# Performance work log

Hardware: AMD Instinct MI355X
Metric: run time of the kernel (lower is better)

Reference implementation:

```python
import jax, jax.numpy as jnp
import numpy as np

N, E = 100000, 3200000
IN, HID, OUT = 512, 256, 64
K, ALPHA = 10, 0.1


def setup_inputs() -> dict:
    key = jax.random.key(0)
    k1, k2, k3, k4, k5, k6 = jax.random.split(key, 6)
    x = jax.random.normal(k1, (N, IN), dtype=jnp.float32)
    edge_index = jax.random.randint(k2, (2, E), 0, N, dtype=jnp.int64)
    s1 = 1.0 / np.sqrt(IN)
    s2 = 1.0 / np.sqrt(HID)
    # nn.Linear default init: U(-1/sqrt(fan_in), 1/sqrt(fan_in))
    W1 = jax.random.uniform(k3, (IN, HID), jnp.float32, -s1, s1)
    b1 = jax.random.uniform(k4, (HID,), jnp.float32, -s1, s1)
    W2 = jax.random.uniform(k5, (HID, OUT), jnp.float32, -s2, s2)
    b2 = jax.random.uniform(k6, (OUT,), jnp.float32, -s2, s2)
    return {"x": x, "edge_index": edge_index, "W1": W1, "b1": b1, "W2": W2, "b2": b2}


def reference(x, edge_index, W1, b1, W2, b2):
    # MLP (dropout is identity in eval mode)
    h = jax.nn.relu(x @ W1 + b1) @ W2 + b2  # [N, OUT]

    # gcn_norm with self-loops (PyG APPNP default, normalize=True)
    loop = jnp.arange(N, dtype=edge_index.dtype)
    src = jnp.concatenate([edge_index[0], loop])  # message sources
    dst = jnp.concatenate([edge_index[1], loop])  # aggregation targets
    deg = jax.ops.segment_sum(jnp.ones_like(dst, dtype=h.dtype), dst, num_segments=N)
    dinv = jnp.where(deg > 0, jax.lax.rsqrt(jnp.maximum(deg, 1.0)), 0.0)
    norm = (dinv[src] * dinv[dst])[:, None]  # [E+N, 1]

    x0 = h
    def step(hk, _):
        agg = jax.ops.segment_sum(norm * hk[src], dst, num_segments=N)
        return (1.0 - ALPHA) * agg + ALPHA * x0, None

    h, _ = jax.lax.scan(step, h, None, length=K)
    return h
```

## Files before the change

### kernel.cpp

```cpp
#include <hip/hip_runtime.h>
#include <hip/hip_bf16.h>

#define IN_F  512
#define HID_F 256
#define OUT_F 64

#define BSHIFT 9
#define BNODES 512
#define NBK_MAX 256
#define EBUF_CAP 18432
#define CURS 16
#define CHUNK 8192

typedef __attribute__((ext_vector_type(8))) short bf16x8;
typedef __attribute__((ext_vector_type(4))) float f32x4;

__device__ inline unsigned short f2bf(float f) {
    unsigned u = __float_as_uint(f);
    u += 0x7FFFu + ((u >> 16) & 1u);
    return (unsigned short)(u >> 16);
}
__device__ inline float bf2f(unsigned v) {
    return __uint_as_float(v << 16);
}

__device__ inline bf16x8 cvt8(f32x4 v0, f32x4 v1) {
    bf16x8 r;
    r[0] = (short)f2bf(v0[0]); r[1] = (short)f2bf(v0[1]);
    r[2] = (short)f2bf(v0[2]); r[3] = (short)f2bf(v0[3]);
    r[4] = (short)f2bf(v1[0]); r[5] = (short)f2bf(v1[1]);
    r[6] = (short)f2bf(v1[2]); r[7] = (short)f2bf(v1[3]);
    return r;
}

__device__ inline void gload_lds16(const void* g, void* l) {
    __builtin_amdgcn_global_load_lds(
        (const __attribute__((address_space(1))) void*)g,
        (__attribute__((address_space(3))) void*)l, 16, 0, 0);
}

__global__ void prep_w_kernel(const float* __restrict__ W1,
                              const float* __restrict__ W2,
                              unsigned short* __restrict__ W1T,
                              unsigned short* __restrict__ W2T)
{
    int i = blockIdx.x * 256 + threadIdx.x;
    if (i < IN_F * HID_F) {
        int k = i / HID_F, n = i % HID_F;
        W1T[n * IN_F + k] = f2bf(W1[i]);
    }
    if (i < HID_F * OUT_F) {
        int k = i / OUT_F, n = i % OUT_F;
        W2T[n * HID_F + k] = f2bf(W2[i]);
    }
}

__global__ __launch_bounds__(512, 4) void mlp_kernel(
    const float* __restrict__ x, const unsigned short* __restrict__ W1T,
    const float* __restrict__ b1, const unsigned short* __restrict__ W2T,
    const float* __restrict__ b2, const float* __restrict__ dinv,
    unsigned short* __restrict__ h0bf, unsigned short* __restrict__ g0, int N)
{
    __shared__ uint4 smem4[4096];
    char* smem = (char*)smem4;

    const int t  = threadIdx.x;
    const int w  = t >> 6;
    const int l  = t & 63;
    const int lr = l & 15;
    const int lq = l >> 4;
    const int wr = w & 3;
    const int wc = w >> 2;

    const int row0 = blockIdx.x * 128;

    f32x4 acc[2][8];
    #pragma unroll
    for (int s = 0; s < 2; ++s)
        #pragma unroll
        for (int f = 0; f < 8; ++f) acc[s][f] = (f32x4){0.f, 0.f, 0.f, 0.f};

    const int ar0 = row0 + wr * 32 + lr;
    const int ar1 = ar0 + 16;
    const bool av0 = ar0 < N, av1 = ar1 < N;
    const float* xp0 = x + (size_t)ar0 * IN_F + lq * 8;
    const float* xp1 = x + (size_t)ar1 * IN_F + lq * 8;

    auto stage = [&](int ks, int buf) {
        #pragma unroll
        for (int is = 0; is < 4; ++is) {
            int j  = is * 512 + t;
            int n  = j >> 3;
            int cs = (j & 7) ^ (n & 7);
            const unsigned short* srcp = W1T + (size_t)n * IN_F + ks * 64 + cs * 8;
            char* dstp = smem + buf * 32768 + is * 8192 + (t >> 6) * 1024;
            gload_lds16(srcp, dstp);
        }
    };

    stage(0, 0);
    __syncthreads();

    for (int ks = 0; ks < 8; ++ks) {
        if (ks < 7) stage(ks + 1, (ks + 1) & 1);
        const char* bb = smem + (ks & 1) * 32768;
        #pragma unroll
        for (int kh = 0; kh < 2; ++kh) {
            const int kofs = ks * 64 + kh * 32;
            bf16x8 a0v, a1v;
            if (av0) {
                a0v = cvt8(*(const f32x4*)(xp0 + kofs),
                           *(const f32x4*)(xp0 + kofs + 4));
            } else {
                #pragma unroll
                for (int j = 0; j < 8; ++j) a0v[j] = 0;
            }
            if (av1) {
                a1v = cvt8(*(const f32x4*)(xp1 + kofs),
                           *(const f32x4*)(xp1 + kofs + 4));
            } else {
                #pragma unroll
                for (int j = 0; j < 8; ++j) a1v[j] = 0;
            }
            #pragma unroll
            for (int f = 0; f < 8; ++f) {
                int n = wc * 128 + f * 16 + lr;
                unsigned off = (unsigned)(n * 128 + kh * 64 + lq * 16);
                bf16x8 b = *(const bf16x8*)(bb + (off ^ ((unsigned)(n & 7) << 4)));
                acc[0][f] = __builtin_amdgcn_mfma_f32_16x16x32_bf16(a0v, b, acc[0][f], 0, 0, 0);
                acc[1][f] = __builtin_amdgcn_mfma_f32_16x16x32_bf16(a1v, b, acc[1][f], 0, 0, 0);
            }
        }
        __syncthreads();
    }

    #pragma unroll
    for (int f = 0; f < 8; ++f) {
        int c = wc * 128 + f * 16 + lr;
        float bbv = b1[c];
        #pragma unroll
        for (int sub = 0; sub < 2; ++sub) {
            #pragma unroll
            for (int j2 = 0; j2 < 4; ++j2) {
                int rr = wr * 32 + sub * 16 + lq * 4 + j2;
                float vv = acc[sub][f][j2] + bbv;
                vv = vv > 0.f ? vv : 0.f;
                unsigned off = (unsigned)(rr * 512 + c * 2);
                *(unsigned short*)(smem + (off ^ ((unsigned)(rr & 7) << 4))) = f2bf(vv);
            }
        }
    }
    __syncthreads();

    const int ct = w & 3;
    const int rh = w >> 2;
    f32x4 a2[4];
    #pragma unroll
    for (int m = 0; m < 4; ++m) a2[m] = (f32x4){0.f, 0.f, 0.f, 0.f};

    const unsigned short* w2p = W2T + (size_t)(ct * 16 + lr) * HID_F + lq * 8;

    #pragma unroll 2
    for (int ks = 0; ks < 8; ++ks) {
        bf16x8 bfrag = *(const bf16x8*)(w2p + ks * 32);
        #pragma unroll
        for (int m = 0; m < 4; ++m) {
            int rr = rh * 64 + m * 16 + lr;
            unsigned off = (unsigned)(rr * 512 + ks * 64 + lq * 16);
            bf16x8 afrag = *(const bf16x8*)(smem + (off ^ ((unsigned)(rr & 7) << 4)));
            a2[m] = __builtin_amdgcn_mfma_f32_16x16x32_bf16(afrag, bfrag, a2[m], 0, 0, 0);
        }
    }

    float bb2 = b2[ct * 16 + lr];
    #pragma unroll
    for (int m = 0; m < 4; ++m) {
        #pragma unroll
        for (int j2 = 0; j2 < 4; ++j2) {
            int rr = row0 + rh * 64 + m * 16 + lq * 4 + j2;
            if (rr < N) {
                float v = a2[m][j2] + bb2;
                int c = ct * 16 + lr;
                h0bf[(size_t)rr * OUT_F + c] = f2bf(v);
                g0[(size_t)rr * OUT_F + c]   = f2bf(dinv[rr] * v);
            }
        }
    }
}

__global__ __launch_bounds__(256) void binned_scatter_kernel(
    const int* __restrict__ src, const int* __restrict__ dst,
    int* __restrict__ bcur, unsigned* __restrict__ ebuf, int E, int nbk)
{
    __shared__ int hist[NBK_MAX];
    __shared__ int gbase[NBK_MAX];
    __shared__ int lcur[NBK_MAX];

    const int t  = threadIdx.x;
    const int bs = blockIdx.x * CHUNK;
    const int nE = min(CHUNK, E - bs);

    if (t < NBK_MAX) { hist[t] = 0; lcur[t] = 0; }
    __syncthreads();

    for (int j = t; j < nE; j += 256)
        atomicAdd(&hist[dst[bs + j] >> BSHIFT], 1);
    __syncthreads();

    for (int b = t; b < nbk; b += 256)
        gbase[b] = hist[b] ? atomicAdd(&bcur[b * CURS], hist[b]) : 0;
    __syncthreads();

    for (int j = t; j < nE; j += 256) {
        int d = dst[bs + j];
        int s = src[bs + j];
        int b = d >> BSHIFT;
        int r = atomicAdd(&lcur[b], 1);
        unsigned pos = (unsigned)(gbase[b] + r);
        if (pos < EBUF_CAP)
            ebuf[(size_t)b * EBUF_CAP + pos] =
                ((unsigned)(d & (BNODES - 1)) << 17) | (unsigned)s;
    }
}

__global__ __launch_bounds__(1024) void bucket_scan_kernel(
    const int* __restrict__ bcur, int* __restrict__ bbase,
    int* __restrict__ off, int nbk, int N, int E)
{
    __shared__ int sm[1024];
    int t = threadIdx.x;
    int v = 0;
    if (t < nbk) {
        v = bcur[t * CURS];
        if (v > EBUF_CAP) v = EBUF_CAP;
    }
    sm[t] = v;
    __syncthreads();
    for (int ofs = 1; ofs < 1024; ofs <<= 1) {
        int x = (t >= ofs) ? sm[t - ofs] : 0;
        __syncthreads();
        sm[t] += x;
        __syncthreads();
    }
    if (t < nbk) bbase[t] = sm[t] - v;
    if (t == nbk - 1) bbase[nbk] = sm[t];
    if (t == 0) off[N] = E;
}

__global__ __launch_bounds__(256) void bucket_build_kernel(
    const unsigned* __restrict__ ebuf, const int* __restrict__ bbase,
    float* __restrict__ dinv, int* __restrict__ off,
    int* __restrict__ csr, int N)
{
    __shared__ int cnt[BNODES];
    __shared__ int loc[BNODES];
    __shared__ int tsum[256];
    const int b = blockIdx.x;
    const int t = threadIdx.x;
    const int beg = bbase[b];
    const int nE  = bbase[b + 1] - beg;
    const unsigned* eb = ebuf + (size_t)b * EBUF_CAP;

    cnt[t] = 0; cnt[t + 256] = 0;
    __syncthreads();
    for (int j = t; j < nE; j += 256)
        atomicAdd(&cnt[eb[j] >> 17], 1);
    __syncthreads();

    int c0 = cnt[2 * t], c1 = cnt[2 * t + 1];
    tsum[t] = c0 + c1;
    __syncthreads();
    for (int ofs = 1; ofs < 256; ofs <<= 1) {
        int v = (t >= ofs) ? tsum[t - ofs] : 0;
        __syncthreads();
        tsum[t] += v;
        __syncthreads();
    }
    int base = (t == 0) ? 0 : tsum[t - 1];
    loc[2 * t]     = beg + base;
    loc[2 * t + 1] = beg + base + c0;
    __syncthreads();

    for (int u = t; u < BNODES; u += 256) {
        int node = b * BNODES + u;
        if (node < N) {
            dinv[node] = rsqrtf((float)(cnt[u] + 1));
            off[node]  = loc[u];
        }
    }
    __syncthreads();
    for (int j = t; j < nE; j += 256) {
        unsigned u = eb[j];
        int pos = atomicAdd(&loc[u >> 17], 1);
        csr[pos] = (int)(u & 0x1FFFFu);
    }
}

__global__ __launch_bounds__(256) void step_kernel(
    const unsigned short* __restrict__ gin,
    const unsigned short* __restrict__ h0bf,
    unsigned short* __restrict__ gout, float* __restrict__ outf,
    const int* __restrict__ off, const int* __restrict__ csr,
    const float* __restrict__ dinv, int N, int last)
{
    const int t    = threadIdx.x;
    const int wid  = (blockIdx.x * 256 + t) >> 6;
    if (wid >= N) return;
    const int lane = t & 63;
    const int es   = lane >> 3;
    const int fb   = lane & 7;

    const uint4* gin4 = (const uint4*)gin;

    float a0 = 0.f, a1 = 0.f, a2 = 0.f, a3 = 0.f;
    float a4 = 0.f, a5 = 0.f, a6 = 0.f, a7 = 0.f;
    const int beg = __builtin_amdgcn_readfirstlane(off[wid]);
    const int end = __builtin_amdgcn_readfirstlane(off[wid + 1]);

    for (int i = beg; i < end; i += 32) {
        int idx[4];
        #pragma unroll
        for (int jj = 0; jj < 4; ++jj) {
            int e = i + jj * 8 + es;
            idx[jj] = (e < end) ? csr[e] : -1;
        }
        uint4 v[4];
        #pragma unroll
        for (int jj = 0; jj < 4; ++jj) {
            v[jj] = (idx[jj] >= 0) ? gin4[(size_t)idx[jj] * 8 + fb]
                                   : make_uint4(0u, 0u, 0u, 0u);
        }
        #pragma unroll
        for (int jj = 0; jj < 4; ++jj) {
            a0 += bf2f(v[jj].x & 0xffffu);
            a1 += bf2f(v[jj].x >> 16);
            a2 += bf2f(v[jj].y & 0xffffu);
            a3 += bf2f(v[jj].y >> 16);
            a4 += bf2f(v[jj].z & 0xffffu);
            a5 += bf2f(v[jj].z >> 16);
            a6 += bf2f(v[jj].w & 0xffffu);
            a7 += bf2f(v[jj].w >> 16);
        }
    }

    a0 += __shfl_xor(a0, 8); a0 += __shfl_xor(a0, 16); a0 += __shfl_xor(a0, 32);
    a1 += __shfl_xor(a1, 8); a1 += __shfl_xor(a1, 16); a1 += __shfl_xor(a1, 32);
    a2 += __shfl_xor(a2, 8); a2 += __shfl_xor(a2, 16); a2 += __shfl_xor(a2, 32);
    a3 += __shfl_xor(a3, 8); a3 += __shfl_xor(a3, 16); a3 += __shfl_xor(a3, 32);
    a4 += __shfl_xor(a4, 8); a4 += __shfl_xor(a4, 16); a4 += __shfl_xor(a4, 32);
    a5 += __shfl_xor(a5, 8); a5 += __shfl_xor(a5, 16); a5 += __shfl_xor(a5, 32);
    a6 += __shfl_xor(a6, 8); a6 += __shfl_xor(a6, 16); a6 += __shfl_xor(a6, 32);
    a7 += __shfl_xor(a7, 8); a7 += __shfl_xor(a7, 16); a7 += __shfl_xor(a7, 32);

    if (es == 0) {
        uint4 sv = gin4[(size_t)wid * 8 + fb];
        uint4 hv = ((const uint4*)h0bf)[(size_t)wid * 8 + fb];
        float dv = dinv[wid];
        float s0 = a0 + bf2f(sv.x & 0xffffu);
        float s1 = a1 + bf2f(sv.x >> 16);
        float s2 = a2 + bf2f(sv.y & 0xffffu);
        float s3 = a3 + bf2f(sv.y >> 16);
        float s4 = a4 + bf2f(sv.z & 0xffffu);
        float s5 = a5 + bf2f(sv.z >> 16);
        float s6 = a6 + bf2f(sv.w & 0xffffu);
        float s7 = a7 + bf2f(sv.w >> 16);
        float r0 = 0.9f * dv * s0 + 0.1f * bf2f(hv.x & 0xffffu);
        float r1 = 0.9f * dv * s1 + 0.1f * bf2f(hv.x >> 16);
        float r2 = 0.9f * dv * s2 + 0.1f * bf2f(hv.y & 0xffffu);
        float r3 = 0.9f * dv * s3 + 0.1f * bf2f(hv.y >> 16);
        float r4 = 0.9f * dv * s4 + 0.1f * bf2f(hv.z & 0xffffu);
        float r5 = 0.9f * dv * s5 + 0.1f * bf2f(hv.z >> 16);
        float r6 = 0.9f * dv * s6 + 0.1f * bf2f(hv.w & 0xffffu);
        float r7 = 0.9f * dv * s7 + 0.1f * bf2f(hv.w >> 16);
        if (last) {
            float* op = outf + (size_t)wid * OUT_F + fb * 8;
            *(float4*)op       = make_float4(r0, r1, r2, r3);
            *(float4*)(op + 4) = make_float4(r4, r5, r6, r7);
        } else {
            uint4 g;
            g.x = (unsigned)f2bf(dv * r0) | ((unsigned)f2bf(dv * r1) << 16);
            g.y = (unsigned)f2bf(dv * r2) | ((unsigned)f2bf(dv * r3) << 16);
            g.z = (unsigned)f2bf(dv * r4) | ((unsigned)f2bf(dv * r5) << 16);
            g.w = (unsigned)f2bf(dv * r6) | ((unsigned)f2bf(dv * r7) << 16);
            ((uint4*)gout)[(size_t)wid * 8 + fb] = g;
        }
    }
}

extern "C" void kernel_launch(void* const* d_in, const int* in_sizes, int n_in,
                              void* d_out, int out_size, void* d_ws, size_t ws_size,
                              hipStream_t stream)
{
    const float* x  = (const float*)d_in[0];
    const int*   ei = (const int*)d_in[1];
    const float* W1 = (const float*)d_in[2];
    const float* b1 = (const float*)d_in[3];
    const float* W2 = (const float*)d_in[4];
    const float* b2 = (const float*)d_in[5];
    float* out = (float*)d_out;

    const int N = in_sizes[0] / IN_F;
    const int E = in_sizes[1] / 2;
    const int* src = ei;
    const int* dst = ei + E;
    const int nbk = (N + BNODES - 1) >> BSHIFT;

    char* wsp = (char*)d_ws;
    auto alloc = [&](size_t bytes) -> char* {
        char* p = wsp;
        wsp += (bytes + 255) & ~(size_t)255;
        return p;
    };
    int*   off  = (int*)  alloc((size_t)(N + 1) * 4);
    float* dinv = (float*)alloc((size_t)N * 4);
    int*   csr  = (int*)  alloc((size_t)E * 4);
    unsigned* ebuf = (unsigned*)alloc((size_t)nbk * EBUF_CAP * 4);
    int*   bcur  = (int*) alloc((size_t)nbk * CURS * 4);
    int*   bbase = (int*) alloc((size_t)(nbk + 1) * 4);
    unsigned short* h0bf = (unsigned short*)alloc((size_t)N * OUT_F * 2);
    unsigned short* gA   = (unsigned short*)alloc((size_t)N * OUT_F * 2);
    unsigned short* gB   = (unsigned short*)alloc((size_t)N * OUT_F * 2);
    unsigned short* W1T  = (unsigned short*)alloc((size_t)IN_F * HID_F * 2);
    unsigned short* W2T  = (unsigned short*)alloc((size_t)HID_F * OUT_F * 2);

    hipMemsetAsync(bcur, 0, (size_t)nbk * CURS * 4, stream);

    const int gScat = (E + CHUNK - 1) / CHUNK;
    binned_scatter_kernel<<<gScat, 256, 0, stream>>>(src, dst, bcur, ebuf, E, nbk);
    bucket_scan_kernel<<<1, 1024, 0, stream>>>(bcur, bbase, off, nbk, N, E);
    bucket_build_kernel<<<nbk, 256, 0, stream>>>(ebuf, bbase, dinv, off, csr, N);

    prep_w_kernel<<<(IN_F * HID_F + 255) / 256, 256, 0, stream>>>(W1, W2, W1T, W2T);
    mlp_kernel<<<(N + 127) / 128, 512, 0, stream>>>(x, W1T, b1, W2T, b2, dinv,
                                                    h0bf, gA, N);

    const int gS = (N + 3) / 4;
    const unsigned short* gin = gA;
    unsigned short* gout = gB;
    for (int k = 0; k < 10; ++k) {
        int last = (k == 9);
        step_kernel<<<gS, 256, 0, stream>>>(gin, h0bf, gout, out, off, csr,
                                            dinv, N, last);
        const unsigned short* tmp = gin;
        gin = gout;
        gout = (unsigned short*)tmp;
    }
}
```

Measured before the change: 765.0 us.

## Stage x tiles through LDS with async loads alongside W1 in first GEMM

The first MLP GEMM used to read x straight from global memory into registers inside the k-loop, while only W1 was staged through LDS. The new code stages both the fp32 x tile and the bf16 W1 tile into double-buffered LDS with asynchronous global-to-LDS loads and swizzled layouts, using a k-step of 32 over 16 iterations. The aim is to overlap the large x stream with MFMA work and hide global load latency. The cost is more barriers, more LDS traffic, and clamped row reads for out-of-range rows in place of zeroing.

Result: faster. 736.0 us (-3.8%).

```diff
diff --git a/kernel.cpp b/kernel.cpp
--- a/kernel.cpp
+++ b/kernel.cpp
@@ -80,56 +80,55 @@
         #pragma unroll
         for (int f = 0; f < 8; ++f) acc[s][f] = (f32x4){0.f, 0.f, 0.f, 0.f};
 
-    const int ar0 = row0 + wr * 32 + lr;
-    const int ar1 = ar0 + 16;
-    const bool av0 = ar0 < N, av1 = ar1 < N;
-    const float* xp0 = x + (size_t)ar0 * IN_F + lq * 8;
-    const float* xp1 = x + (size_t)ar1 * IN_F + lq * 8;
-
-    auto stage = [&](int ks, int buf) {
-        #pragma unroll
-        for (int is = 0; is < 4; ++is) {
-            int j  = is * 512 + t;
-            int n  = j >> 3;
-            int cs = (j & 7) ^ (n & 7);
-            const unsigned short* srcp = W1T + (size_t)n * IN_F + ks * 64 + cs * 8;
-            char* dstp = smem + buf * 32768 + is * 8192 + (t >> 6) * 1024;
+    auto stageX = [&](int ks, int buf) {
+        #pragma unroll
+        for (int is = 0; is < 2; ++is) {
+            int j = is * 512 + t;
+            int r = j >> 3;
+            int c = j & 7;
+            int gr = row0 + r; if (gr > N - 1) gr = N - 1;
+            const float* srcp = x + (size_t)gr * IN_F + ks * 32 + ((c ^ (r & 7)) << 2);
+            char* dstp = smem + buf * 16384 + is * 8192 + (t >> 6) * 1024;
             gload_lds16(srcp, dstp);
         }
     };
-
-    stage(0, 0);
-    __syncthreads();
-
-    for (int ks = 0; ks < 8; ++ks) {
-        if (ks < 7) stage(ks + 1, (ks + 1) & 1);
-        const char* bb = smem + (ks & 1) * 32768;
-        #pragma unroll
-        for (int kh = 0; kh < 2; ++kh) {
-            const int kofs = ks * 64 + kh * 32;
-            bf16x8 a0v, a1v;
-            if (av0) {
-                a0v = cvt8(*(const f32x4*)(xp0 + kofs),
-                           *(const f32x4*)(xp0 + kofs + 4));
-            } else {
-                #pragma unroll
-                for (int j = 0; j < 8; ++j) a0v[j] = 0;
-            }
-            if (av1) {
-                a1v = cvt8(*(const f32x4*)(xp1 + kofs),
-                           *(const f32x4*)(xp1 + kofs + 4));
-            } else {
-                #pragma unroll
-                for (int j = 0; j < 8; ++j) a1v[j] = 0;
-            }
-            #pragma unroll
-            for (int f = 0; f < 8; ++f) {
-                int n = wc * 128 + f * 16 + lr;
-                unsigned off = (unsigned)(n * 128 + kh * 64 + lq * 16);
-                bf16x8 b = *(const bf16x8*)(bb + (off ^ ((unsigned)(n & 7) << 4)));
-                acc[0][f] = __builtin_amdgcn_mfma_f32_16x16x32_bf16(a0v, b, acc[0][f], 0, 0, 0);
-                acc[1][f] = __builtin_amdgcn_mfma_f32_16x16x32_bf16(a1v, b, acc[1][f], 0, 0, 0);
-            }
+    auto stageB = [&](int ks, int buf) {
+        #pragma unroll
+        for (int is = 0; is < 2; ++is) {
+            int j = is * 512 + t;
+            int n = j >> 2;
+            int c = j & 3;
+            const unsigned short* srcp = W1T + (size_t)n * IN_F + ks * 32 + ((c ^ (n & 3)) << 3);
+            char* dstp = smem + 32768 + buf * 16384 + is * 8192 + (t >> 6) * 1024;
+            gload_lds16(srcp, dstp);
+        }
+    };
+
+    stageX(0, 0); stageB(0, 0);
+    __syncthreads();
+
+    const int r0 = wr * 32 + lr;
+    const int r1 = r0 + 16;
+    const int sw = r0 & 7;
+
+    for (int ks = 0; ks < 16; ++ks) {
+        if (ks < 15) { stageX(ks + 1, (ks + 1) & 1); stageB(ks + 1, (ks + 1) & 1); }
+        const char* xb = smem + (ks & 1) * 16384;
+        const char* bbuf = smem + 32768 + (ks & 1) * 16384;
+
+        f32x4 u0 = *(const f32x4*)(xb + r0 * 128 + (((2 * lq)     ^ sw) << 4));
+        f32x4 u1 = *(const f32x4*)(xb + r0 * 128 + (((2 * lq + 1) ^ sw) << 4));
+        f32x4 u2 = *(const f32x4*)(xb + r1 * 128 + (((2 * lq)     ^ sw) << 4));
+        f32x4 u3 = *(const f32x4*)(xb + r1 * 128 + (((2 * lq + 1) ^ sw) << 4));
+        bf16x8 a0v = cvt8(u0, u1);
+        bf16x8 a1v = cvt8(u2, u3);
+
+        #pragma unroll
+        for (int f = 0; f < 8; ++f) {
+            int n = wc * 128 + f * 16 + lr;
+            bf16x8 b = *(const bf16x8*)(bbuf + n * 64 + ((lq ^ (n & 3)) << 4));
+            acc[0][f] = __builtin_amdgcn_mfma_f32_16x16x32_bf16(a0v, b, acc[0][f], 0, 0, 0);
+            acc[1][f] = __builtin_amdgcn_mfma_f32_16x16x32_bf16(a1v, b, acc[1][f], 0, 0, 0);
         }
         __syncthreads();
     }
```
